# Performance work log

Measured on AMD Instinct MI355X. Metric: run time of the kernel, lower is better.

The kernel has to match this reference:

```python
import jax, jax.numpy as jnp
import numpy as np
from jax import lax

GRID = 16
NUM_UNITS = 10
N_UNITS = NUM_UNITS * 2
UNIT_OBS_SIZE = 32
GRID_OBS_SIZE = GRID * GRID + N_UNITS * 10 + 2  # 458
OBS_SIZE = GRID_OBS_SIZE + UNIT_OBS_SIZE        # 490
ACTION_SIZE = 16
B = 16384
CNN_FEATURES = 256
UNIT_FEATURES = 64
TRUNK_FEATURES = 256


def setup_inputs() -> dict:
    key = jax.random.key(0)
    ks = jax.random.split(key, 24)
    obs = jax.random.uniform(ks[0], (B, OBS_SIZE), dtype=jnp.float32)
    # Distinct cell per unit per sample -> scatter-add == serial set semantics.
    n_cells = (GRID - 1) * (GRID - 1)
    cells = jnp.argsort(jax.random.uniform(ks[1], (B, n_cells)), axis=-1)[:, :N_UNITS]
    r = (cells // (GRID - 1)).astype(jnp.float32) / (GRID - 1)
    c = (cells % (GRID - 1)).astype(jnp.float32) / (GRID - 1)
    base = GRID * GRID
    uidx = jnp.arange(N_UNITS)
    obs = obs.at[:, base + uidx * 10 + 2].set(r).at[:, base + uidx * 10 + 3].set(c)

    def w(k, shape, s=0.1):
        return jax.random.normal(k, shape, dtype=jnp.float32) * s

    return {
        "obs": obs,
        "conv1_w": w(ks[2], (32, 9, 3, 3)), "conv1_b": jnp.zeros((32,), jnp.float32),
        "conv2_w": w(ks[3], (64, 32, 3, 3)), "conv2_b": jnp.zeros((64,), jnp.float32),
        "conv3_w": w(ks[4], (64, 64, 3, 3)), "conv3_b": jnp.zeros((64,), jnp.float32),
        "fc_w": w(ks[5], (CNN_FEATURES, 64 * 4 * 4)), "fc_b": jnp.zeros((CNN_FEATURES,), jnp.float32),
        "u1_w": w(ks[6], (64, UNIT_OBS_SIZE)), "u1_b": jnp.zeros((64,), jnp.float32),
        "u2_w": w(ks[7], (UNIT_FEATURES, 64)), "u2_b": jnp.zeros((UNIT_FEATURES,), jnp.float32),
        "t1_w": w(ks[8], (TRUNK_FEATURES, CNN_FEATURES + UNIT_FEATURES)), "t1_b": jnp.zeros((TRUNK_FEATURES,), jnp.float32),
        "t2_w": w(ks[9], (TRUNK_FEATURES, TRUNK_FEATURES)), "t2_b": jnp.zeros((TRUNK_FEATURES,), jnp.float32),
        "actor_w": w(ks[10], (ACTION_SIZE, TRUNK_FEATURES), 0.01), "actor_b": jnp.zeros((ACTION_SIZE,), jnp.float32),
        "critic_w": w(ks[11], (1, TRUNK_FEATURES)), "critic_b": jnp.zeros((1,), jnp.float32),
    }


def _preprocess(obs):
    Bn = obs.shape[0]
    terrain = obs[:, :GRID * GRID].reshape(Bn, 1, GRID, GRID)
    units = obs[:, GRID * GRID:GRID * GRID + N_UNITS * 10].reshape(Bn, N_UNITS, 10)
    unit_obs = obs[:, GRID_OBS_SIZE:]
    team = units[..., 1]
    r = (units[..., 2] * (GRID - 1)).astype(jnp.int32)
    c = (units[..., 3] * (GRID - 1)).astype(jnp.int32)
    hp = units[..., 4]
    moved = units[..., 5]
    acted = units[..., 6]
    alive = hp > 0
    blue = team < 0.5
    flat = r * GRID + c                       # (B, N_UNITS)
    bidx = jnp.arange(Bn)[:, None]

    def scat(vals, mask):
        z = jnp.zeros((Bn, GRID * GRID), obs.dtype)
        z = z.at[bidx, flat].add(jnp.where(mask, vals, 0.0))
        return z.reshape(Bn, 1, GRID, GRID)

    ones = jnp.ones_like(hp)
    mb = alive & blue
    mr = alive & ~blue
    grid = jnp.concatenate([
        terrain,
        scat(ones, mb), scat(ones, mr),
        scat(hp, mb), scat(hp, mr),
        scat(moved, mb), scat(acted, mb),
        scat(moved, mr), scat(acted, mr),
    ], axis=1)                                # (B, 9, 16, 16)
    return grid, unit_obs


def _conv(x, w, b):
    y = lax.conv_general_dilated(x, w, (1, 1), 'SAME',
                                 dimension_numbers=('NCHW', 'OIHW', 'NCHW'))
    return jax.nn.relu(y + b[None, :, None, None])


def _lin(x, w, b):
    return x @ w.T + b


def reference(obs, conv1_w, conv1_b, conv2_w, conv2_b, conv3_w, conv3_b,
              fc_w, fc_b, u1_w, u1_b, u2_w, u2_b, t1_w, t1_b, t2_w, t2_b,
              actor_w, actor_b, critic_w, critic_b):
    grid, unit = _preprocess(obs)
    x = _conv(grid, conv1_w, conv1_b)
    x = _conv(x, conv2_w, conv2_b)
    x = _conv(x, conv3_w, conv3_b)            # (B, 64, 16, 16)
    # AdaptiveAvgPool2d((4,4)) on 16x16 == 4x4 mean pooling
    Bn = x.shape[0]
    x = x.reshape(Bn, 64, 4, 4, 4, 4).mean(axis=(3, 5))
    x = x.reshape(Bn, 64 * 4 * 4)
    cnn_feat = jax.nn.relu(_lin(x, fc_w, fc_b))
    uh = jax.nn.relu(_lin(unit, u1_w, u1_b))
    unit_feat = jax.nn.relu(_lin(uh, u2_w, u2_b))
    t = jnp.concatenate([cnn_feat, unit_feat], axis=-1)
    t = jax.nn.relu(_lin(t, t1_w, t1_b))
    t = jax.nn.relu(_lin(t, t2_w, t2_b))
    logits = _lin(t, actor_w, actor_b)        # (B, ACTION_SIZE)
    value = _lin(t, critic_w, critic_b)       # (B, 1)
    return logits, value
```

## Files before the change

### kernel.cpp

```cpp
#include <hip/hip_runtime.h>

#define OBS_STRIDE 490

typedef _Float16 half8 __attribute__((ext_vector_type(8)));
typedef _Float16 half4 __attribute__((ext_vector_type(4)));
typedef float f32x4 __attribute__((ext_vector_type(4)));

union H8 { half8 h; uint4 u; };

#define FC_BASE 126
#define T1_BASE 638
#define T2_BASE 798
#define HD_BASE 926
#define NFRAG   942

__global__ __launch_bounds__(256) void prep_weights(
    const float* __restrict__ w1, const float* __restrict__ w2,
    const float* __restrict__ w3,
    const float* __restrict__ fcw, const float* __restrict__ t1w,
    const float* __restrict__ t2w,
    const float* __restrict__ aw,  const float* __restrict__ cw,
    uint4* __restrict__ wfrag)
{
    int gid = blockIdx.x * 256 + threadIdx.x;
    if (gid >= NFRAG * 64) return;
    int fid = gid >> 6, lane = gid & 63;
    H8 v;
    if (fid < 126) {
        const float* W; int C, sh, kt, mt;
        if (fid < 18)      { int f = fid;      W = w1; C = 9;  sh = f >> 1; kt = 0;            mt = f & 1; }
        else if (fid < 54) { int f = fid - 18; W = w2; C = 32; sh = f >> 2; kt = 0;            mt = f & 3; }
        else               { int f = fid - 54; W = w3; C = 64; sh = f >> 3; kt = (f >> 2) & 1; mt = f & 3; }
        int o  = mt * 16 + (lane & 15);
        int c0 = kt * 32 + ((lane >> 4) << 3);
        #pragma unroll
        for (int i = 0; i < 8; ++i) {
            int c = c0 + i;
            v.h[i] = (c < C) ? (_Float16)W[(o * C + c) * 9 + sh] : (_Float16)0.f;
        }
    } else {
        int o16 = lane & 15, k0 = (lane >> 4) << 3;
        if (fid < HD_BASE) {
            const float* W; int K, f;
            if (fid < T1_BASE)      { f = fid - FC_BASE; W = fcw; K = 1024; }
            else if (fid < T2_BASE) { f = fid - T1_BASE; W = t1w; K = 320;  }
            else                    { f = fid - T2_BASE; W = t2w; K = 256;  }
            int ks = f >> 4, mtg = f & 15;
            int o = mtg * 16 + o16;
            int kb = ks * 32 + k0;
            #pragma unroll
            for (int i = 0; i < 8; ++i)
                v.h[i] = (_Float16)W[(size_t)o * K + kb + i];
        } else {
            int f = fid - HD_BASE;
            int ks = f >> 1, mtg = f & 1;
            int kb = ks * 32 + k0;
            #pragma unroll
            for (int i = 0; i < 8; ++i) {
                float x;
                if (mtg == 0)      x = aw[o16 * 256 + kb + i];
                else if (o16 == 0) x = cw[kb + i];
                else               x = 0.f;
                v.h[i] = (_Float16)x;
            }
        }
    }
    wfrag[gid] = v.u;
}

template<int KT, int MT, int FRAG_BASE>
__device__ __forceinline__ void conv_layer(
    unsigned char* Abuf, const uint4* __restrict__ wfrag,
    const float* __restrict__ bias, int lane, int wv)
{
    const int x = lane & 15;
    const int q = lane >> 4;
    f32x4 acc[4][MT];
    #pragma unroll
    for (int mt = 0; mt < MT; ++mt) {
        f32x4 bv = *(const f32x4*)(bias + mt * 16 + q * 4);
        #pragma unroll
        for (int row = 0; row < 4; ++row) acc[row][mt] = bv;
    }
    #pragma unroll
    for (int sh = 0; sh < 9; ++sh) {
        const int dy = sh / 3 - 1, dx = sh % 3 - 1;
        const int xs = x + dx + 1;
        #pragma unroll
        for (int kt = 0; kt < KT; ++kt) {
            H8 wf[MT];
            #pragma unroll
            for (int mt = 0; mt < MT; ++mt)
                wf[mt].u = wfrag[(FRAG_BASE + (sh * KT + kt) * MT + mt) * 64 + lane];
            const int chunk = ((kt * 4 + q) ^ (xs & 7)) << 4;
            #pragma unroll
            for (int row = 0; row < 4; ++row) {
                const int ys = wv * 4 + row + dy + 1;
                if (ys >= 1 && ys <= 16) {
                    half8 bf = *(const half8*)(Abuf + (ys - 1) * 2304 + xs * 128 + chunk);
                    #pragma unroll
                    for (int mt = 0; mt < MT; ++mt)
                        acc[row][mt] = __builtin_amdgcn_mfma_f32_16x16x32_f16(
                            wf[mt].h, bf, acc[row][mt], 0, 0, 0);
                }
            }
        }
    }
    __syncthreads();
    const int xs1 = x + 1;
    #pragma unroll
    for (int row = 0; row < 4; ++row) {
        const int yi = wv * 4 + row;
        #pragma unroll
        for (int mt = 0; mt < MT; ++mt) {
            half4 hv;
            #pragma unroll
            for (int r = 0; r < 4; ++r) hv[r] = (_Float16)fmaxf(acc[row][mt][r], 0.f);
            const int ob = mt * 32 + q * 8;
            const int addr = yi * 2304 + xs1 * 128 + ((((ob >> 4) ^ (xs1 & 7))) << 4) + (ob & 15);
            *(half4*)(Abuf + addr) = hv;
        }
    }
    __syncthreads();
}

__global__ __launch_bounds__(256, 4) void conv_kernel(
    const float* __restrict__ obs,
    const uint4* __restrict__ wfrag,
    const float* __restrict__ b1, const float* __restrict__ b2,
    const float* __restrict__ b3,
    _Float16* __restrict__ pooled)
{
    __shared__ alignas(16) unsigned char Abuf[16 * 18 * 128];

    const int tid = threadIdx.x;
    const int b = blockIdx.x;
    const float* ob = obs + (size_t)b * OBS_STRIDE;

    {
        uint4* A4 = (uint4*)Abuf;
        #pragma unroll
        for (int it = 0; it < 9; ++it) {
            int i = tid + it * 256;
            int r0 = i / 144;
            int rem = i - r0 * 144;
            int xs = rem >> 3, pc = rem & 7;
            int c = pc ^ (xs & 7);
            uint4 v = {0, 0, 0, 0};
            if (c == 0 && xs >= 1 && xs <= 16) {
                H8 h;
                #pragma unroll
                for (int j = 0; j < 8; ++j) h.h[j] = (_Float16)0.f;
                h.h[0] = (_Float16)ob[r0 * 16 + xs - 1];
                v = h.u;
            }
            A4[i] = v;
        }
    }
    __syncthreads();

    if (tid < 20) {
        const float* up = ob + 256 + tid * 10;
        float team = up[1], rf = up[2], cf = up[3];
        float hp = up[4], mv = up[5], ac = up[6];
        if (hp > 0.f) {
            int r = (int)(rf * 15.f), c = (int)(cf * 15.f);
            const unsigned base = (unsigned)(r * 2304 + (c + 1) * 128);
            const int sw = (c + 1) & 7;
#define SCAT_W(CH, VAL) { const int obyte = (CH) * 2;                                   \
        *(_Float16*)(Abuf + base + ((((obyte >> 4) ^ sw)) << 4) + (obyte & 15)) =       \
            (_Float16)(VAL); }
            if (team < 0.5f) {
                SCAT_W(1, 1.f) SCAT_W(3, hp) SCAT_W(5, mv) SCAT_W(6, ac)
            } else {
                SCAT_W(2, 1.f) SCAT_W(4, hp) SCAT_W(7, mv) SCAT_W(8, ac)
            }
#undef SCAT_W
        }
    }
    __syncthreads();

    const int lane = tid & 63, wv = tid >> 6;
    conv_layer<1, 2, 0 >(Abuf, wfrag, b1, lane, wv);
    conv_layer<1, 4, 18>(Abuf, wfrag, b2, lane, wv);
    conv_layer<2, 4, 54>(Abuf, wfrag, b3, lane, wv);

    {
        int qq = tid & 15, cg = tid >> 4;
        int ph = qq >> 2, pw = qq & 3;
        int ch0 = cg * 4;
        float s[4] = {0.f, 0.f, 0.f, 0.f};
        int ob2 = ch0 * 2;
        #pragma unroll
        for (int dy = 0; dy < 4; ++dy) {
            int yi = ph * 4 + dy;
            #pragma unroll
            for (int dx = 0; dx < 4; ++dx) {
                int xs = pw * 4 + dx + 1;
                int addr = yi * 2304 + xs * 128 + ((((ob2 >> 4) ^ (xs & 7))) << 4) + (ob2 & 15);
                half4 hv = *(const half4*)(Abuf + addr);
                #pragma unroll
                for (int cc = 0; cc < 4; ++cc) s[cc] += (float)hv[cc];
            }
        }
        _Float16* pb = pooled + (size_t)b * 1024;
        #pragma unroll
        for (int cc = 0; cc < 4; ++cc)
            pb[(ch0 + cc) * 16 + qq] = (_Float16)(s[cc] * 0.0625f);
    }
}

__global__ __launch_bounds__(256) void tail_kernel(
    const float* __restrict__ obs,
    const _Float16* __restrict__ pooled,
    const uint4* __restrict__ wfrag,
    const float* __restrict__ fcb,
    const float* __restrict__ u1w, const float* __restrict__ u1b,
    const float* __restrict__ u2w, const float* __restrict__ u2b,
    const float* __restrict__ t1b, const float* __restrict__ t2b,
    const float* __restrict__ ab,  const float* __restrict__ cb,
    float* __restrict__ out, int NB)
{
    __shared__ alignas(16) _Float16 tcT[32][344];
    __shared__ alignas(16) _Float16 uh[32][72];

    const int tid  = threadIdx.x;
    const int lane = tid & 63, w = tid >> 6;
    const int nl   = lane & 15, q = lane >> 4;
    const int r0   = blockIdx.x * 32;

    {
        const int r = tid >> 3, t8 = tid & 7;
        const float* up = obs + (size_t)(r0 + r) * OBS_STRIDE + 458;
        float xin[32];
        #pragma unroll
        for (int k2 = 0; k2 < 16; ++k2) {
            float2 v = *(const float2*)(up + k2 * 2);
            xin[k2 * 2] = v.x; xin[k2 * 2 + 1] = v.y;
        }
        #pragma unroll
        for (int oo = 0; oo < 8; ++oo) {
            int o = t8 * 8 + oo;
            float a = u1b[o];
            const float* wr = u1w + o * 32;
            #pragma unroll
            for (int k = 0; k < 32; ++k) a = fmaf(xin[k], wr[k], a);
            uh[r][o] = (_Float16)fmaxf(a, 0.f);
        }
    }
    __syncthreads();

    {
        const int r = tid >> 3, t8 = tid & 7;
        float xin[64];
        #pragma unroll
        for (int k8 = 0; k8 < 8; ++k8) {
            half8 v = *(const half8*)&uh[r][k8 * 8];
            #pragma unroll
            for (int j = 0; j < 8; ++j) xin[k8 * 8 + j] = (float)v[j];
        }
        #pragma unroll
        for (int oo = 0; oo < 8; ++oo) {
            int o = t8 * 8 + oo;
            float a = u2b[o];
            const float* wr = u2w + o * 64;
            #pragma unroll
            for (int k = 0; k < 64; ++k) a = fmaf(xin[k], wr[k], a);
            tcT[r][256 + o] = (_Float16)fmaxf(a, 0.f);
        }
    }

    {
        f32x4 acc[4][2];
        #pragma unroll
        for (int mt = 0; mt < 4; ++mt) {
            f32x4 bv = *(const f32x4*)(fcb + (w * 4 + mt) * 16 + q * 4);
            acc[mt][0] = bv; acc[mt][1] = bv;
        }
        for (int ks = 0; ks < 32; ++ks) {
            H8 bf[2];
            #pragma unroll
            for (int g = 0; g < 2; ++g)
                bf[g].u = *(const uint4*)(pooled + (size_t)(r0 + g * 16 + nl) * 1024 + ks * 32 + q * 8);
            #pragma unroll
            for (int mt = 0; mt < 4; ++mt) {
                H8 af; af.u = wfrag[(size_t)(FC_BASE + ks * 16 + w * 4 + mt) * 64 + lane];
                #pragma unroll
                for (int g = 0; g < 2; ++g)
                    acc[mt][g] = __builtin_amdgcn_mfma_f32_16x16x32_f16(af.h, bf[g].h, acc[mt][g], 0, 0, 0);
            }
        }
        #pragma unroll
        for (int mt = 0; mt < 4; ++mt)
            #pragma unroll
            for (int g = 0; g < 2; ++g) {
                half4 hv;
                #pragma unroll
                for (int r = 0; r < 4; ++r) hv[r] = (_Float16)fmaxf(acc[mt][g][r], 0.f);
                *(half4*)&tcT[g * 16 + nl][(w * 4 + mt) * 16 + q * 4] = hv;
            }
    }
    __syncthreads();

    {
        f32x4 acc[4][2];
        #pragma unroll
        for (int mt = 0; mt < 4; ++mt) {
            f32x4 bv = *(const f32x4*)(t1b + (w * 4 + mt) * 16 + q * 4);
            acc[mt][0] = bv; acc[mt][1] = bv;
        }
        for (int ks = 0; ks < 10; ++ks) {
            H8 bf[2];
            #pragma unroll
            for (int g = 0; g < 2; ++g)
                bf[g].h = *(const half8*)&tcT[g * 16 + nl][ks * 32 + q * 8];
            #pragma unroll
            for (int mt = 0; mt < 4; ++mt) {
                H8 af; af.u = wfrag[(size_t)(T1_BASE + ks * 16 + w * 4 + mt) * 64 + lane];
                #pragma unroll
                for (int g = 0; g < 2; ++g)
                    acc[mt][g] = __builtin_amdgcn_mfma_f32_16x16x32_f16(af.h, bf[g].h, acc[mt][g], 0, 0, 0);
            }
        }
        __syncthreads();
        #pragma unroll
        for (int mt = 0; mt < 4; ++mt)
            #pragma unroll
            for (int g = 0; g < 2; ++g) {
                half4 hv;
                #pragma unroll
                for (int r = 0; r < 4; ++r) hv[r] = (_Float16)fmaxf(acc[mt][g][r], 0.f);
                *(half4*)&tcT[g * 16 + nl][(w * 4 + mt) * 16 + q * 4] = hv;
            }
    }
    __syncthreads();

    {
        f32x4 acc[4][2];
        #pragma unroll
        for (int mt = 0; mt < 4; ++mt) {
            f32x4 bv = *(const f32x4*)(t2b + (w * 4 + mt) * 16 + q * 4);
            acc[mt][0] = bv; acc[mt][1] = bv;
        }
        for (int ks = 0; ks < 8; ++ks) {
            H8 bf[2];
            #pragma unroll
            for (int g = 0; g < 2; ++g)
                bf[g].h = *(const half8*)&tcT[g * 16 + nl][ks * 32 + q * 8];
            #pragma unroll
            for (int mt = 0; mt < 4; ++mt) {
                H8 af; af.u = wfrag[(size_t)(T2_BASE + ks * 16 + w * 4 + mt) * 64 + lane];
                #pragma unroll
                for (int g = 0; g < 2; ++g)
                    acc[mt][g] = __builtin_amdgcn_mfma_f32_16x16x32_f16(af.h, bf[g].h, acc[mt][g], 0, 0, 0);
            }
        }
        __syncthreads();
        #pragma unroll
        for (int mt = 0; mt < 4; ++mt)
            #pragma unroll
            for (int g = 0; g < 2; ++g) {
                half4 hv;
                #pragma unroll
                for (int r = 0; r < 4; ++r) hv[r] = (_Float16)fmaxf(acc[mt][g][r], 0.f);
                *(half4*)&tcT[g * 16 + nl][(w * 4 + mt) * 16 + q * 4] = hv;
            }
    }
    __syncthreads();

    if (w < 2) {
        f32x4 acc[2];
        if (w == 0) {
            f32x4 bv = *(const f32x4*)(ab + q * 4);
            acc[0] = bv; acc[1] = bv;
        } else {
            f32x4 bv = {0.f, 0.f, 0.f, 0.f};
            if (q == 0) bv[0] = cb[0];
            acc[0] = bv; acc[1] = bv;
        }
        for (int ks = 0; ks < 8; ++ks) {
            H8 af; af.u = wfrag[(size_t)(HD_BASE + ks * 2 + w) * 64 + lane];
            #pragma unroll
            for (int g = 0; g < 2; ++g) {
                half8 bf = *(const half8*)&tcT[g * 16 + nl][ks * 32 + q * 8];
                acc[g] = __builtin_amdgcn_mfma_f32_16x16x32_f16(af.h, bf, acc[g], 0, 0, 0);
            }
        }
        if (w == 0) {
            #pragma unroll
            for (int g = 0; g < 2; ++g) {
                float4 o4 = {acc[g][0], acc[g][1], acc[g][2], acc[g][3]};
                *(float4*)(out + (size_t)(r0 + g * 16 + nl) * 16 + q * 4) = o4;
            }
        } else if (q == 0) {
            #pragma unroll
            for (int g = 0; g < 2; ++g)
                out[(size_t)NB * 16 + r0 + g * 16 + nl] = acc[g][0];
        }
    }
}

extern "C" void kernel_launch(void* const* d_in, const int* in_sizes, int n_in,
                              void* d_out, int out_size, void* d_ws, size_t ws_size,
                              hipStream_t stream)
{
    const float* obs = (const float*)d_in[0];
    const float* w1  = (const float*)d_in[1];
    const float* b1  = (const float*)d_in[2];
    const float* w2  = (const float*)d_in[3];
    const float* b2  = (const float*)d_in[4];
    const float* w3  = (const float*)d_in[5];
    const float* b3  = (const float*)d_in[6];
    const float* fcw = (const float*)d_in[7];
    const float* fcb = (const float*)d_in[8];
    const float* u1w = (const float*)d_in[9];
    const float* u1b = (const float*)d_in[10];
    const float* u2w = (const float*)d_in[11];
    const float* u2b = (const float*)d_in[12];
    const float* t1w = (const float*)d_in[13];
    const float* t1b = (const float*)d_in[14];
    const float* t2w = (const float*)d_in[15];
    const float* t2b = (const float*)d_in[16];
    const float* aw  = (const float*)d_in[17];
    const float* ab  = (const float*)d_in[18];
    const float* cw  = (const float*)d_in[19];
    const float* cb  = (const float*)d_in[20];

    const int NB = in_sizes[0] / OBS_STRIDE;
    _Float16* pooled = (_Float16*)d_ws;
    uint4* wfrag = (uint4*)((char*)d_ws + (size_t)NB * 1024 * 2);

    prep_weights<<<(NFRAG * 64 + 255) / 256, 256, 0, stream>>>(
        w1, w2, w3, fcw, t1w, t2w, aw, cw, wfrag);
    conv_kernel<<<NB, 256, 0, stream>>>(obs, (const uint4*)wfrag, b1, b2, b3, pooled);
    tail_kernel<<<NB / 32, 256, 0, stream>>>(obs, pooled, (const uint4*)wfrag,
                                             fcb, u1w, u1b, u2w, u2b,
                                             t1b, t2b, ab, cb,
                                             (float*)d_out, NB);
}
```

Before: 565.0 us.

## Use 32x32x16 MFMA conv tiles with two images per block

The conv layers switch from 16x16x32 MFMA to 32x32x16 MFMA. Each block now processes two images with 512 threads, and the two images' pixels are packed into the 32-wide N dimension. The shared-memory layout drops the halo padding and handles x-boundaries with predicated zero loads, using a new swizzle that includes the image index. The aim is to halve weight-fragment reloads per image and raise MFMA efficiency, at the cost of higher register use per thread and a larger block.

After: 644.9 us. 1.14x slower.

```diff
diff --git a/kernel.cpp b/kernel.cpp
--- a/kernel.cpp
+++ b/kernel.cpp
@@ -5,14 +5,19 @@
 typedef _Float16 half8 __attribute__((ext_vector_type(8)));
 typedef _Float16 half4 __attribute__((ext_vector_type(4)));
 typedef float f32x4 __attribute__((ext_vector_type(4)));
+typedef float f32x16 __attribute__((ext_vector_type(16)));
 
 union H8 { half8 h; uint4 u; };
 
-#define FC_BASE 126
-#define T1_BASE 638
-#define T2_BASE 798
-#define HD_BASE 926
-#define NFRAG   942
+#define C2_BASE 9
+#define C3_BASE 45
+#define FC_BASE 117
+#define T1_BASE 629
+#define T2_BASE 789
+#define HD_BASE 917
+#define NFRAG   933
+
+#define CSWZ(xs, img) ((((xs) & 7) ^ ((((xs) >> 3) & 1) << 1)) ^ ((img) << 2))
 
 __global__ __launch_bounds__(256) void prep_weights(
     const float* __restrict__ w1, const float* __restrict__ w2,
@@ -26,13 +31,13 @@
     if (gid >= NFRAG * 64) return;
     int fid = gid >> 6, lane = gid & 63;
     H8 v;
-    if (fid < 126) {
+    if (fid < FC_BASE) {
         const float* W; int C, sh, kt, mt;
-        if (fid < 18)      { int f = fid;      W = w1; C = 9;  sh = f >> 1; kt = 0;            mt = f & 1; }
-        else if (fid < 54) { int f = fid - 18; W = w2; C = 32; sh = f >> 2; kt = 0;            mt = f & 3; }
-        else               { int f = fid - 54; W = w3; C = 64; sh = f >> 3; kt = (f >> 2) & 1; mt = f & 3; }
-        int o  = mt * 16 + (lane & 15);
-        int c0 = kt * 32 + ((lane >> 4) << 3);
+        if (fid < C2_BASE)      { W = w1; C = 9;  sh = fid; kt = 0; mt = 0; }
+        else if (fid < C3_BASE) { int f = fid - C2_BASE; W = w2; C = 32; sh = f >> 2; kt = (f >> 1) & 1; mt = f & 1; }
+        else                    { int f = fid - C3_BASE; W = w3; C = 64; sh = f >> 3; kt = (f >> 1) & 3; mt = f & 1; }
+        int o  = mt * 32 + (lane & 31);
+        int c0 = kt * 16 + ((lane >> 5) << 3);
         #pragma unroll
         for (int i = 0; i < 8; ++i) {
             int c = c0 + i;
@@ -68,90 +73,109 @@
     wfrag[gid] = v.u;
 }
 
-template<int KT, int MT, int FRAG_BASE>
-__device__ __forceinline__ void conv_layer(
+template<int KT, int MT, int BASE>
+__device__ __forceinline__ void conv_layer32(
     unsigned char* Abuf, const uint4* __restrict__ wfrag,
-    const float* __restrict__ bias, int lane, int wv)
+    const float* __restrict__ bias, int lane, int w)
 {
-    const int x = lane & 15;
-    const int q = lane >> 4;
-    f32x4 acc[4][MT];
+    const int x   = lane & 15;
+    const int img = (lane >> 4) & 1;
+    const int kg  = lane >> 5;
+    const unsigned ibase = (unsigned)img * 32768u;
+
+    f32x16 acc[2][MT];
     #pragma unroll
     for (int mt = 0; mt < MT; ++mt) {
-        f32x4 bv = *(const f32x4*)(bias + mt * 16 + q * 4);
-        #pragma unroll
-        for (int row = 0; row < 4; ++row) acc[row][mt] = bv;
-    }
+        f32x16 bv;
+        #pragma unroll
+        for (int g2 = 0; g2 < 4; ++g2) {
+            f32x4 b4 = *(const f32x4*)(bias + mt * 32 + g2 * 8 + kg * 4);
+            #pragma unroll
+            for (int j = 0; j < 4; ++j) bv[g2 * 4 + j] = b4[j];
+        }
+        acc[0][mt] = bv;
+        acc[1][mt] = bv;
+    }
+
     #pragma unroll
     for (int sh = 0; sh < 9; ++sh) {
         const int dy = sh / 3 - 1, dx = sh % 3 - 1;
-        const int xs = x + dx + 1;
+        const int xsr = x + dx;
+        const bool xok = (xsr >= 0) && (xsr <= 15);
         #pragma unroll
         for (int kt = 0; kt < KT; ++kt) {
             H8 wf[MT];
             #pragma unroll
             for (int mt = 0; mt < MT; ++mt)
-                wf[mt].u = wfrag[(FRAG_BASE + (sh * KT + kt) * MT + mt) * 64 + lane];
-            const int chunk = ((kt * 4 + q) ^ (xs & 7)) << 4;
-            #pragma unroll
-            for (int row = 0; row < 4; ++row) {
-                const int ys = wv * 4 + row + dy + 1;
-                if (ys >= 1 && ys <= 16) {
-                    half8 bf = *(const half8*)(Abuf + (ys - 1) * 2304 + xs * 128 + chunk);
+                wf[mt].u = wfrag[(BASE + (sh * KT + kt) * MT + mt) * 64 + lane];
+            const unsigned coff = (unsigned)(((kt * 2 + kg) ^ CSWZ(xsr & 15, img)) << 4);
+            #pragma unroll
+            for (int rt = 0; rt < 2; ++rt) {
+                const int ys = w * 2 + rt + dy;
+                if (ys >= 0 && ys <= 15) {
+                    H8 bf; bf.u = make_uint4(0u, 0u, 0u, 0u);
+                    if (xok)
+                        bf.u = *(const uint4*)(Abuf + ibase + (unsigned)ys * 2048u
+                                               + (unsigned)xsr * 128u + coff);
                     #pragma unroll
                     for (int mt = 0; mt < MT; ++mt)
-                        acc[row][mt] = __builtin_amdgcn_mfma_f32_16x16x32_f16(
-                            wf[mt].h, bf, acc[row][mt], 0, 0, 0);
+                        acc[rt][mt] = __builtin_amdgcn_mfma_f32_32x32x16_f16(
+                            wf[mt].h, bf.h, acc[rt][mt], 0, 0, 0);
                 }
             }
         }
     }
-    __syncthreads();
-    const int xs1 = x + 1;
+
+    __syncthreads();
     #pragma unroll
-    for (int row = 0; row < 4; ++row) {
-        const int yi = wv * 4 + row;
-        #pragma unroll
-        for (int mt = 0; mt < MT; ++mt) {
-            half4 hv;
-            #pragma unroll
-            for (int r = 0; r < 4; ++r) hv[r] = (_Float16)fmaxf(acc[row][mt][r], 0.f);
-            const int ob = mt * 32 + q * 8;
-            const int addr = yi * 2304 + xs1 * 128 + ((((ob >> 4) ^ (xs1 & 7))) << 4) + (ob & 15);
-            *(half4*)(Abuf + addr) = hv;
-        }
+    for (int rt = 0; rt < 2; ++rt) {
+        const int row = w * 2 + rt;
+        #pragma unroll
+        for (int mt = 0; mt < MT; ++mt)
+            #pragma unroll
+            for (int g2 = 0; g2 < 4; ++g2) {
+                half4 hv;
+                #pragma unroll
+                for (int j = 0; j < 4; ++j)
+                    hv[j] = (_Float16)fmaxf(acc[rt][mt][g2 * 4 + j], 0.f);
+                const int c0 = mt * 32 + g2 * 8 + kg * 4;
+                const unsigned addr = ibase + (unsigned)row * 2048u + (unsigned)x * 128u
+                    + (unsigned)((((c0 >> 3) ^ CSWZ(x, img)) << 4) + ((c0 & 7) * 2));
+                *(half4*)(Abuf + addr) = hv;
+            }
     }
     __syncthreads();
 }
 
-__global__ __launch_bounds__(256, 4) void conv_kernel(
+__global__ __launch_bounds__(512, 4) void conv_kernel(
     const float* __restrict__ obs,
     const uint4* __restrict__ wfrag,
     const float* __restrict__ b1, const float* __restrict__ b2,
     const float* __restrict__ b3,
     _Float16* __restrict__ pooled)
 {
-    __shared__ alignas(16) unsigned char Abuf[16 * 18 * 128];
+    __shared__ alignas(16) unsigned char Abuf[2 * 16 * 16 * 128];
 
     const int tid = threadIdx.x;
-    const int b = blockIdx.x;
-    const float* ob = obs + (size_t)b * OBS_STRIDE;
+    const int bb  = blockIdx.x;
 
     {
         uint4* A4 = (uint4*)Abuf;
         #pragma unroll
-        for (int it = 0; it < 9; ++it) {
-            int i = tid + it * 256;
-            int r0 = i / 144;
-            int rem = i - r0 * 144;
+        for (int it = 0; it < 8; ++it) {
+            int i = tid + it * 512;
+            int img = i >> 11;
+            int j = i & 2047;
+            int r0 = j >> 7;
+            int rem = j & 127;
             int xs = rem >> 3, pc = rem & 7;
-            int c = pc ^ (xs & 7);
+            int c = pc ^ CSWZ(xs, img);
             uint4 v = {0, 0, 0, 0};
-            if (c == 0 && xs >= 1 && xs <= 16) {
+            if (c == 0) {
                 H8 h;
                 #pragma unroll
-                for (int j = 0; j < 8; ++j) h.h[j] = (_Float16)0.f;
-                h.h[0] = (_Float16)ob[r0 * 16 + xs - 1];
+                for (int k = 0; k < 8; ++k) h.h[k] = (_Float16)0.f;
+                h.h[0] = (_Float16)obs[(size_t)(bb * 2 + img) * OBS_STRIDE + r0 * 16 + xs];
                 v = h.u;
             }
             A4[i] = v;
@@ -159,14 +183,16 @@
     }
     __syncthreads();
 
-    if (tid < 20) {
-        const float* up = ob + 256 + tid * 10;
+    if (tid < 40) {
+        int img = tid >= 20 ? 1 : 0;
+        int u = tid - img * 20;
+        const float* up = obs + (size_t)(bb * 2 + img) * OBS_STRIDE + 256 + u * 10;
         float team = up[1], rf = up[2], cf = up[3];
         float hp = up[4], mv = up[5], ac = up[6];
         if (hp > 0.f) {
             int r = (int)(rf * 15.f), c = (int)(cf * 15.f);
-            const unsigned base = (unsigned)(r * 2304 + (c + 1) * 128);
-            const int sw = (c + 1) & 7;
+            const unsigned base = (unsigned)img * 32768u + (unsigned)r * 2048u + (unsigned)c * 128u;
+            const int sw = CSWZ(c, img);
 #define SCAT_W(CH, VAL) { const int obyte = (CH) * 2;                                   \
         *(_Float16*)(Abuf + base + ((((obyte >> 4) ^ sw)) << 4) + (obyte & 15)) =       \
             (_Float16)(VAL); }
@@ -180,30 +206,31 @@
     }
     __syncthreads();
 
-    const int lane = tid & 63, wv = tid >> 6;
-    conv_layer<1, 2, 0 >(Abuf, wfrag, b1, lane, wv);
-    conv_layer<1, 4, 18>(Abuf, wfrag, b2, lane, wv);
-    conv_layer<2, 4, 54>(Abuf, wfrag, b3, lane, wv);
-
-    {
-        int qq = tid & 15, cg = tid >> 4;
+    const int lane = tid & 63, w = tid >> 6;
+    conv_layer32<1, 1, 0      >(Abuf, wfrag, b1, lane, w);
+    conv_layer32<2, 2, C2_BASE>(Abuf, wfrag, b2, lane, w);
+    conv_layer32<4, 2, C3_BASE>(Abuf, wfrag, b3, lane, w);
+
+    {
+        int img = tid >> 8, t = tid & 255;
+        int qq = t & 15, cg = t >> 4;
         int ph = qq >> 2, pw = qq & 3;
-        int ch0 = cg * 4;
+        int ch0 = cg * 4, ob2 = ch0 * 2;
         float s[4] = {0.f, 0.f, 0.f, 0.f};
-        int ob2 = ch0 * 2;
         #pragma unroll
         for (int dy = 0; dy < 4; ++dy) {
             int yi = ph * 4 + dy;
             #pragma unroll
             for (int dx = 0; dx < 4; ++dx) {
-                int xs = pw * 4 + dx + 1;
-                int addr = yi * 2304 + xs * 128 + ((((ob2 >> 4) ^ (xs & 7))) << 4) + (ob2 & 15);
+                int xs = pw * 4 + dx;
+                unsigned addr = (unsigned)img * 32768u + (unsigned)yi * 2048u + (unsigned)xs * 128u
+                    + (unsigned)((((ob2 >> 4) ^ CSWZ(xs, img)) << 4) + (ob2 & 15));
                 half4 hv = *(const half4*)(Abuf + addr);
                 #pragma unroll
                 for (int cc = 0; cc < 4; ++cc) s[cc] += (float)hv[cc];
             }
         }
-        _Float16* pb = pooled + (size_t)b * 1024;
+        _Float16* pb = pooled + (size_t)(bb * 2 + img) * 1024;
         #pragma unroll
         for (int cc = 0; cc < 4; ++cc)
             pb[(ch0 + cc) * 16 + qq] = (_Float16)(s[cc] * 0.0625f);
@@ -432,7 +459,7 @@
 
     prep_weights<<<(NFRAG * 64 + 255) / 256, 256, 0, stream>>>(
         w1, w2, w3, fcw, t1w, t2w, aw, cw, wfrag);
-    conv_kernel<<<NB, 256, 0, stream>>>(obs, (const uint4*)wfrag, b1, b2, b3, pooled);
+    conv_kernel<<<NB / 2, 512, 0, stream>>>(obs, (const uint4*)wfrag, b1, b2, b3, pooled);
     tail_kernel<<<NB / 32, 256, 0, stream>>>(obs, pooled, (const uint4*)wfrag,
                                              fcb, u1w, u1b, u2w, u2b,
                                              t1b, t2b, ab, cb,
```
